# Kernel tuning notes

Measured on AMD Instinct MI355X. Metric: run time of the kernel, lower is better.

## Reference

```python
import jax, jax.numpy as jnp
import numpy as np

HIDDEN = 1024
INTER = 4096


def setup_inputs() -> dict:
    key = jax.random.key(0)
    k1, k2, k3, k4, k5 = jax.random.split(key, 5)
    hidden_states = jax.random.normal(k1, (4, 4096, HIDDEN), dtype=jnp.float32)
    # nn.Linear stores weight as [out, in]; we keep that convention.
    W1 = jax.random.normal(k2, (INTER, HIDDEN), dtype=jnp.float32) * (1.0 / np.sqrt(HIDDEN))
    b1 = jax.random.normal(k3, (INTER,), dtype=jnp.float32) * 0.01
    W2 = jax.random.normal(k4, (HIDDEN, INTER), dtype=jnp.float32) * (1.0 / np.sqrt(INTER))
    b2 = jax.random.normal(k5, (HIDDEN,), dtype=jnp.float32) * 0.01
    return {"hidden_states": hidden_states, "W1": W1, "b1": b1, "W2": W2, "b2": b2}


def reference(hidden_states, W1, b1, W2, b2):
    # secure_matmul(x, W.T) + secure_add(bias)  ->  x @ W1.T + b1
    inter = jnp.einsum('bsh,fh->bsf', hidden_states, W1) + b1
    # secure_relu
    act = jax.nn.relu(inter)
    # second secure linear projection
    out = jnp.einsum('bsf,hf->bsh', act, W2) + b2
    return out
```

## Files before the change

kernel.cpp:

```cpp
#include <hip/hip_runtime.h>
#include <cstdint>
#include <cstddef>


typedef __bf16 bf16x8 __attribute__((ext_vector_type(8)));
typedef float f32x4 __attribute__((ext_vector_type(4)));

__device__ __forceinline__ unsigned short f32_to_bf16_rn(float f) {
  union { float f; unsigned int u; } v; v.f = f;
  unsigned int u = v.u;
  u += 0x7fffu + ((u >> 16) & 1u);
  return (unsigned short)(u >> 16);
}

__global__ void cvt_f32_bf16(const float* __restrict__ in,
                             unsigned short* __restrict__ out, int n4) {
  int i = blockIdx.x * blockDim.x + threadIdx.x;
  const int stride = gridDim.x * blockDim.x;
  for (; i < n4; i += stride) {
    const float4 v = reinterpret_cast<const float4*>(in)[i];
    ushort4 o;
    o.x = f32_to_bf16_rn(v.x);
    o.y = f32_to_bf16_rn(v.y);
    o.z = f32_to_bf16_rn(v.z);
    o.w = f32_to_bf16_rn(v.w);
    reinterpret_cast<ushort4*>(out)[i] = o;
  }
}

__device__ __forceinline__ void gload_lds16(const void* g, void* l) {
  __builtin_amdgcn_global_load_lds(
      (const __attribute__((address_space(1))) void*)g,
      (__attribute__((address_space(3))) void*)l,
      16, 0, 0);
}

#define VMCNT6 asm volatile("s_waitcnt vmcnt(6)" ::: "memory")
#define LGKMCNT0 asm volatile("s_waitcnt lgkmcnt(0)" ::: "memory")

#define APL(BUF, KH) (((BUF)*2 + (KH)) * 16384)
#define BPL(BUF, KH) (65536 + ((BUF)*2 + (KH)) * 16384)

#define STAGE(PLANEOFF, GROW, KB) do {                                          \
    gload_lds16((GROW) + (size_t)srow0 * pitch + (KB) + scol0,                  \
                lds + (PLANEOFF) + ldsw0);                                      \
    gload_lds16((GROW) + (size_t)srow1 * pitch + (KB) + scol1,                  \
                lds + (PLANEOFF) + ldsw1);                                      \
  } while (0)

#define PHASE(BUF, QK, QN, LOADA, STAGE_STMT, DOVM) do {                        \
    const unsigned char* pA_ = lds + APL(BUF, QK) + wroff + alane;              \
    const unsigned char* pB_ = lds + BPL(BUF, QK) + wcoff + alane;              \
    if (LOADA) {                                                                \
      _Pragma("unroll") for (int m_ = 0; m_ < 8; ++m_)                          \
        af[m_] = *(const bf16x8*)(pA_ + (m_ << 10));                            \
    }                                                                           \
    bfr[0] = *(const bf16x8*)(pB_ + (((QN)*2 + 0) << 10));                      \
    bfr[1] = *(const bf16x8*)(pB_ + (((QN)*2 + 1) << 10));                      \
    STAGE_STMT;                                                                 \
    __builtin_amdgcn_s_barrier();                                               \
    LGKMCNT0;                                                                   \
    __builtin_amdgcn_sched_barrier(0);                                          \
    __builtin_amdgcn_s_setprio(1);                                              \
    _Pragma("unroll") for (int m_ = 0; m_ < 8; ++m_) {                          \
      acc[m_][(QN)*2 + 0] = __builtin_amdgcn_mfma_f32_16x16x32_bf16(            \
          af[m_], bfr[0], acc[m_][(QN)*2 + 0], 0, 0, 0);                        \
      acc[m_][(QN)*2 + 1] = __builtin_amdgcn_mfma_f32_16x16x32_bf16(            \
          af[m_], bfr[1], acc[m_][(QN)*2 + 1], 0, 0, 0);                        \
    }                                                                           \
    __builtin_amdgcn_s_setprio(0);                                              \
    if (DOVM) { VMCNT6; }                                                       \
    __builtin_amdgcn_s_barrier();                                               \
    __builtin_amdgcn_sched_barrier(0);                                          \
  } while (0)

template <int RELU_BF16_OUT, int NBN>
__global__ __launch_bounds__(512, 2) void gemm8(
    const unsigned short* __restrict__ A,
    const unsigned short* __restrict__ B,
    const float* __restrict__ bias,
    void* __restrict__ Cout,
    int K) {
  constexpr int N = NBN * 256;
  __shared__ unsigned char lds[131072];

  const int tid = threadIdx.x;
  const int l = tid & 63;
  const int w = tid >> 6;
  const int wr = w >> 2;
  const int wc = w & 3;

  const int nwg = gridDim.x;
  const int cpx = nwg >> 3;
  const int bid = blockIdx.x;
  const int swz = (bid & 7) * cpx + (bid >> 3);
  const int bmi = swz / NBN;
  const int bni = swz % NBN;

  const size_t pitch = (size_t)K * 2;
  const char* Ag = (const char*)A + (size_t)(bmi << 8) * pitch;
  const char* Bg = (const char*)B + (size_t)(bni << 8) * pitch;

  const int sd0 = tid << 4;
  const int sd1 = sd0 + 8192;
  const int srow0 = sd0 >> 6;
  const int srow1 = sd1 >> 6;
  const int scol0 = (sd0 & 63) ^ (((sd0 >> 7) & 3) << 4);
  const int scol1 = (sd1 & 63) ^ (((sd1 >> 7) & 3) << 4);
  const int ldsw0 = (w << 10);
  const int ldsw1 = 8192 + (w << 10);

  const int alane = ((l & 15) << 6) + (((l >> 4) << 4) ^ (((l >> 1) & 3) << 4));
  const int wroff = wr << 13;
  const int wcoff = wc << 12;

  f32x4 acc[8][4];
#pragma unroll
  for (int m = 0; m < 8; ++m)
#pragma unroll
    for (int n = 0; n < 4; ++n) { f32x4 z = 0.f; acc[m][n] = z; }
  bf16x8 af[8];
  bf16x8 bfr[2];

  const int nt = K >> 6;

  STAGE(APL(0, 0), Ag, 0);
  STAGE(BPL(0, 0), Bg, 0);
  STAGE(APL(0, 1), Ag, 64);
  STAGE(BPL(0, 1), Bg, 64);
  STAGE(APL(1, 0), Ag, 128);
  STAGE(BPL(1, 0), Bg, 128);
  STAGE(APL(1, 1), Ag, 192);
  VMCNT6;
  __builtin_amdgcn_s_barrier();

  for (int it = 0; it < (nt >> 1); ++it) {
    const int t1 = 2 * it + 1;
    int t2 = 2 * it + 2; if (t2 >= nt) t2 = nt - 1;
    int t3 = 2 * it + 3; if (t3 >= nt) t3 = nt - 1;
    const int kb1 = t1 << 7;
    const int kb2 = t2 << 7;
    const int kb3 = t3 << 7;

    PHASE(0, 0, 0, 1, STAGE(BPL(1, 1), Bg, kb1 + 64), 0);
    PHASE(0, 0, 1, 0, STAGE(APL(0, 0), Ag, kb2), 1);
    PHASE(0, 1, 0, 1, STAGE(BPL(0, 0), Bg, kb2), 0);
    PHASE(0, 1, 1, 0, STAGE(APL(0, 1), Ag, kb2 + 64), 1);
    PHASE(1, 0, 0, 1, STAGE(BPL(0, 1), Bg, kb2 + 64), 0);
    PHASE(1, 0, 1, 0, STAGE(APL(1, 0), Ag, kb3), 1);
    PHASE(1, 1, 0, 1, STAGE(BPL(1, 0), Bg, kb3), 0);
    PHASE(1, 1, 1, 0, STAGE(APL(1, 1), Ag, kb3 + 64), 1);
  }

  const int crow0 = (bmi << 8) + (wr << 7) + ((l >> 4) << 2);
  const int ccol0 = (bni << 8) + (wc << 6) + (l & 15);
  if (RELU_BF16_OUT) {
    unsigned short* C = (unsigned short*)Cout;
#pragma unroll
    for (int n = 0; n < 4; ++n) {
      const int col = ccol0 + (n << 4);
      const float bv = bias[col];
#pragma unroll
      for (int m = 0; m < 8; ++m) {
#pragma unroll
        for (int r = 0; r < 4; ++r) {
          float v = acc[m][n][r] + bv;
          v = fmaxf(v, 0.0f);
          C[(size_t)(crow0 + (m << 4) + r) * N + col] = f32_to_bf16_rn(v);
        }
      }
    }
  } else {
    float* C = (float*)Cout;
#pragma unroll
    for (int n = 0; n < 4; ++n) {
      const int col = ccol0 + (n << 4);
      const float bv = bias[col];
#pragma unroll
      for (int m = 0; m < 8; ++m) {
#pragma unroll
        for (int r = 0; r < 4; ++r) {
          C[(size_t)(crow0 + (m << 4) + r) * N + col] = acc[m][n][r] + bv;
        }
      }
    }
  }
}

extern "C" void kernel_launch(void* const* d_in, const int* in_sizes, int n_in,
                              void* d_out, int out_size, void* d_ws, size_t ws_size,
                              hipStream_t stream) {
  const float* x  = (const float*)d_in[0];
  const float* W1 = (const float*)d_in[1];
  const float* b1 = (const float*)d_in[2];
  const float* W2 = (const float*)d_in[3];
  const float* b2 = (const float*)d_in[4];
  float* out = (float*)d_out;

  const int M = 16384, H = 1024, F = 4096;

  unsigned short* xb  = (unsigned short*)d_ws;
  unsigned short* w1b = xb + (size_t)M * H;
  unsigned short* w2b = w1b + (size_t)F * H;
  unsigned short* act = w2b + (size_t)H * F;

  cvt_f32_bf16<<<4096, 256, 0, stream>>>(x, xb, (M * H) / 4);
  cvt_f32_bf16<<<1024, 256, 0, stream>>>(W1, w1b, (F * H) / 4);
  cvt_f32_bf16<<<1024, 256, 0, stream>>>(W2, w2b, (H * F) / 4);

  gemm8<1, 16><<<dim3((M / 256) * (F / 256)), 512, 0, stream>>>(xb, w1b, b1, act, H);
  gemm8<0, 4><<<dim3((M / 256) * (H / 256)), 512, 0, stream>>>(act, w2b, b2, out, F);
}
```

Before: 421.8 us.

## Merge conversion kernels, reorder LDS fragment loads, and stage ReLU epilogue through LDS

Merges the three fp32-to-bf16 conversion launches into one grid-stride kernel, which removes launch overhead. The GEMM phase loads B fragments before A and drops the explicit lgkmcnt wait before the barrier, leaving that wait to the compiler. The first GEMM's bias+ReLU epilogue now transposes tiles through per-wave LDS so each lane writes 8-byte ushort4 rows instead of scattered 2-byte stores. The epilogue adds LDS round trips, and removing LGKMCNT0 relies on compiler-inserted waits being correct.

```diff
diff --git a/kernel.cpp b/kernel.cpp
--- a/kernel.cpp
+++ b/kernel.cpp
@@ -13,18 +13,28 @@
   return (unsigned short)(u >> 16);
 }
 
-__global__ void cvt_f32_bf16(const float* __restrict__ in,
-                             unsigned short* __restrict__ out, int n4) {
+__global__ void cvt_all(const float* __restrict__ x,
+                        const float* __restrict__ w1,
+                        const float* __restrict__ w2,
+                        unsigned short* __restrict__ xb,
+                        unsigned short* __restrict__ w1b,
+                        unsigned short* __restrict__ w2b,
+                        int nx4, int nw4) {
+  const int stride = gridDim.x * blockDim.x;
   int i = blockIdx.x * blockDim.x + threadIdx.x;
-  const int stride = gridDim.x * blockDim.x;
-  for (; i < n4; i += stride) {
-    const float4 v = reinterpret_cast<const float4*>(in)[i];
+  const int total = nx4 + 2 * nw4;
+  for (; i < total; i += stride) {
+    const float* src; unsigned short* dst; int j;
+    if (i < nx4) { src = x; dst = xb; j = i; }
+    else if (i < nx4 + nw4) { src = w1; dst = w1b; j = i - nx4; }
+    else { src = w2; dst = w2b; j = i - nx4 - nw4; }
+    const float4 v = reinterpret_cast<const float4*>(src)[j];
     ushort4 o;
     o.x = f32_to_bf16_rn(v.x);
     o.y = f32_to_bf16_rn(v.y);
     o.z = f32_to_bf16_rn(v.z);
     o.w = f32_to_bf16_rn(v.w);
-    reinterpret_cast<ushort4*>(out)[i] = o;
+    reinterpret_cast<ushort4*>(dst)[j] = o;
   }
 }
 
@@ -36,6 +46,7 @@
 }
 
 #define VMCNT6 asm volatile("s_waitcnt vmcnt(6)" ::: "memory")
+#define VMCNT0 asm volatile("s_waitcnt vmcnt(0)" ::: "memory")
 #define LGKMCNT0 asm volatile("s_waitcnt lgkmcnt(0)" ::: "memory")
 
 #define APL(BUF, KH) (((BUF)*2 + (KH)) * 16384)
@@ -51,15 +62,15 @@
 #define PHASE(BUF, QK, QN, LOADA, STAGE_STMT, DOVM) do {                        \
     const unsigned char* pA_ = lds + APL(BUF, QK) + wroff + alane;              \
     const unsigned char* pB_ = lds + BPL(BUF, QK) + wcoff + alane;              \
+    bfr[0] = *(const bf16x8*)(pB_ + (((QN)*2 + 0) << 10));                      \
+    bfr[1] = *(const bf16x8*)(pB_ + (((QN)*2 + 1) << 10));                      \
     if (LOADA) {                                                                \
       _Pragma("unroll") for (int m_ = 0; m_ < 8; ++m_)                          \
         af[m_] = *(const bf16x8*)(pA_ + (m_ << 10));                            \
     }                                                                           \
-    bfr[0] = *(const bf16x8*)(pB_ + (((QN)*2 + 0) << 10));                      \
-    bfr[1] = *(const bf16x8*)(pB_ + (((QN)*2 + 1) << 10));                      \
     STAGE_STMT;                                                                 \
+    __builtin_amdgcn_sched_barrier(0);                                          \
     __builtin_amdgcn_s_barrier();                                               \
-    LGKMCNT0;                                                                   \
     __builtin_amdgcn_sched_barrier(0);                                          \
     __builtin_amdgcn_s_setprio(1);                                              \
     _Pragma("unroll") for (int m_ = 0; m_ < 8; ++m_) {                          \
@@ -70,8 +81,8 @@
     }                                                                           \
     __builtin_amdgcn_s_setprio(0);                                              \
     if (DOVM) { VMCNT6; }                                                       \
+    __builtin_amdgcn_sched_barrier(0);                                          \
     __builtin_amdgcn_s_barrier();                                               \
-    __builtin_amdgcn_sched_barrier(0);                                          \
   } while (0)
 
 template <int RELU_BF16_OUT, int NBN>
@@ -154,21 +165,48 @@
 
   const int crow0 = (bmi << 8) + (wr << 7) + ((l >> 4) << 2);
   const int ccol0 = (bni << 8) + (wc << 6) + (l & 15);
+
   if (RELU_BF16_OUT) {
+    VMCNT0;
+    __builtin_amdgcn_s_barrier();
+    float bv[4];
+#pragma unroll
+    for (int n = 0; n < 4; ++n) bv[n] = bias[ccol0 + (n << 4)];
     unsigned short* C = (unsigned short*)Cout;
-#pragma unroll
-    for (int n = 0; n < 4; ++n) {
-      const int col = ccol0 + (n << 4);
-      const float bv = bias[col];
-#pragma unroll
-      for (int m = 0; m < 8; ++m) {
-#pragma unroll
-        for (int r = 0; r < 4; ++r) {
-          float v = acc[m][n][r] + bv;
-          v = fmaxf(v, 0.0f);
-          C[(size_t)(crow0 + (m << 4) + r) * N + col] = f32_to_bf16_rn(v);
+    unsigned char* myl = lds + w * 9216;
+    const int lw = l & 15;
+    const int lg = l >> 4;
+    for (int mp = 0; mp < 4; ++mp) {
+#pragma unroll
+      for (int m2 = 0; m2 < 2; ++m2) {
+        const int m = mp * 2 + m2;
+#pragma unroll
+        for (int n = 0; n < 4; ++n) {
+#pragma unroll
+          for (int r = 0; r < 4; ++r) {
+            const float v = fmaxf(acc[m][n][r] + bv[n], 0.0f);
+            const int row = m2 * 16 + lg * 4 + r;
+            *(float*)(myl + row * 288 + ((n * 16 + lw) << 2)) = v;
+          }
         }
       }
+      LGKMCNT0;
+      __builtin_amdgcn_sched_barrier(0);
+#pragma unroll
+      for (int k = 0; k < 8; ++k) {
+        const int row = k * 4 + lg;
+        const float4 t = *(const float4*)(myl + row * 288 + (lw << 4));
+        ushort4 o;
+        o.x = f32_to_bf16_rn(t.x);
+        o.y = f32_to_bf16_rn(t.y);
+        o.z = f32_to_bf16_rn(t.z);
+        o.w = f32_to_bf16_rn(t.w);
+        const int grow = (bmi << 8) + (wr << 7) + (mp << 5) + row;
+        const int gcol = (bni << 8) + (wc << 6) + (lw << 2);
+        *(ushort4*)(C + (size_t)grow * N + gcol) = o;
+      }
+      LGKMCNT0;
+      __builtin_amdgcn_sched_barrier(0);
     }
   } else {
     float* C = (float*)Cout;
@@ -204,9 +242,8 @@
   unsigned short* w2b = w1b + (size_t)F * H;
   unsigned short* act = w2b + (size_t)H * F;
 
-  cvt_f32_bf16<<<4096, 256, 0, stream>>>(x, xb, (M * H) / 4);
-  cvt_f32_bf16<<<1024, 256, 0, stream>>>(W1, w1b, (F * H) / 4);
-  cvt_f32_bf16<<<1024, 256, 0, stream>>>(W2, w2b, (H * F) / 4);
+  cvt_all<<<2048, 256, 0, stream>>>(x, W1, W2, xb, w1b, w2b,
+                                    (M * H) / 4, (F * H) / 4);
 
   gemm8<1, 16><<<dim3((M / 256) * (F / 256)), 512, 0, stream>>>(xb, w1b, b1, act, H);
   gemm8<0, 4><<<dim3((M / 256) * (H / 256)), 512, 0, stream>>>(act, w2b, b2, out, F);
```

After: 395.5 us. 6.2% less time.
